# Kernel tuning notes

Measured on AMD Instinct MI355X. Metric: run time of the kernel, lower is better.

Reference implementation:

```python
import jax, jax.numpy as jnp
import numpy as np

NUM_HEADS = 10
LN_EPS = 1e-5


def setup_inputs() -> dict:
    key = jax.random.key(0)
    ks = jax.random.split(key, 6)
    N, D = 4096, 640  # in_dim == out_dim required by residual add
    x = jax.random.normal(ks[0], (N, D), dtype=jnp.float32)
    s = 1.0 / np.sqrt(D)
    Wq = jax.random.normal(ks[1], (D, D), dtype=jnp.float32) * s  # torch Linear weight [out,in]
    Wk = jax.random.normal(ks[2], (D, D), dtype=jnp.float32) * s
    Wv = jax.random.normal(ks[3], (D, D), dtype=jnp.float32) * s
    gamma = jnp.ones((D,), dtype=jnp.float32)
    beta = jnp.zeros((D,), dtype=jnp.float32)
    return {"x": x, "Wq": Wq, "Wk": Wk, "Wv": Wv, "gamma": gamma, "beta": beta}


def reference(x, Wq, Wk, Wv, gamma, beta):
    N, D = x.shape
    dk = D // NUM_HEADS
    Q = x @ Wq.T  # [N, D]
    K = x @ Wk.T
    V = x @ Wv.T
    # Faithful to source: raw reshapes (NOT transposes)
    Qh = Q.reshape(NUM_HEADS, N, dk)
    Kh = K.reshape(NUM_HEADS, N, dk).reshape(NUM_HEADS, dk, N)  # torch.reshape, not .mT
    Vh = V.reshape(NUM_HEADS, N, dk)
    # Faithful quirk: scale by sqrt(K.shape[2]) == sqrt(N)
    scale = np.float32(np.sqrt(N))
    wghts = jax.nn.softmax((Qh @ Kh) / scale, axis=-1)  # [H, N, N]
    values = wghts @ Vh  # [H, N, dk]
    values = values.reshape(N, NUM_HEADS * dk)  # raw reshape merge
    values = values + x  # residual
    # LayerNorm(out_dim), biased variance, eps=1e-5
    mean = jnp.mean(values, axis=-1, keepdims=True)
    var = jnp.mean(jnp.square(values - mean), axis=-1, keepdims=True)
    out = (values - mean) * jax.lax.rsqrt(var + LN_EPS) * gamma + beta
    return out
```

## Files before the change

kernel.cpp:

```cpp
#include <hip/hip_runtime.h>
#if __has_include(<hip/hip_fp8.h>)
#include <hip/hip_fp8.h>
#endif


typedef __bf16 bf16x8 __attribute__((ext_vector_type(8)));
typedef __bf16 bf16x4 __attribute__((ext_vector_type(4)));
typedef float  f32x4  __attribute__((ext_vector_type(4)));
typedef unsigned short u16x4 __attribute__((ext_vector_type(4)));
typedef unsigned int   u32x4 __attribute__((ext_vector_type(4)));

#define N_TOK   4096
#define D_MODEL 640
#define DK      64
#define HSLAB   (N_TOK * DK)
#define SQS 0.15014030f

#if __has_builtin(__builtin_amdgcn_exp2f)
#define EXP2(x) __builtin_amdgcn_exp2f(x)
#else
#define EXP2(x) exp2f(x)
#endif

__device__ __forceinline__ void stage16(const void* g, void* lds_uniform) {
    __builtin_amdgcn_global_load_lds(
        (const __attribute__((address_space(1))) unsigned int*)g,
        (__attribute__((address_space(3))) unsigned int*)lds_uniform, 16, 0, 0);
}

__device__ __forceinline__ u16x4 cvt4(f32x4 v) {
    return __builtin_bit_cast(u16x4, __builtin_convertvector(v, bf16x4));
}

__device__ __forceinline__ unsigned int pk_fp8(f32x4 v) {
#if __has_builtin(__builtin_amdgcn_cvt_pk_fp8_f32)
    int r = 0;
    r = __builtin_amdgcn_cvt_pk_fp8_f32(v[0], v[1], r, false);
    r = __builtin_amdgcn_cvt_pk_fp8_f32(v[2], v[3], r, true);
    return (unsigned int)r;
#else
    union { unsigned char b[4]; unsigned int u; } x;
    x.b[0] = __hip_fp8_e4m3(v[0]).__x;
    x.b[1] = __hip_fp8_e4m3(v[1]).__x;
    x.b[2] = __hip_fp8_e4m3(v[2]).__x;
    x.b[3] = __hip_fp8_e4m3(v[3]).__x;
    return x.u;
#endif
}

__global__ __launch_bounds__(256) void cvt_all(const float* __restrict__ x,
                                               const float* __restrict__ w0,
                                               const float* __restrict__ w1,
                                               const float* __restrict__ w2,
                                               unsigned short* __restrict__ xb,
                                               unsigned short* __restrict__ d0,
                                               unsigned short* __restrict__ d1,
                                               unsigned short* __restrict__ d2,
                                               f32x4* __restrict__ ltot4) {
    int i = blockIdx.x * 256 + threadIdx.x;
    if (i >= 962560) { ltot4[i - 962560] = (f32x4){0.f, 0.f, 0.f, 0.f}; return; }
    const float* s; unsigned short* d; int off; float scl = 1.0f;
    if (i < 655360) { s = x; d = xb; off = i; }
    else {
        int j = i - 655360;
        int w = j / 102400; off = j - w * 102400;
        s = (w == 0) ? w0 : (w == 1) ? w1 : w2;
        d = (w == 0) ? d0 : (w == 1) ? d1 : d2;
        if (w < 2) scl = SQS;
    }
    f32x4 v = ((const f32x4*)s)[off];
    v[0] *= scl; v[1] *= scl; v[2] *= scl; v[3] *= scl;
    ((u16x4*)d)[off] = cvt4(v);
}

__global__ __launch_bounds__(256, 2) void gemm_qkv(
    const unsigned short* __restrict__ xb,
    const unsigned short* __restrict__ wq,
    const unsigned short* __restrict__ wk,
    const unsigned short* __restrict__ wv,
    unsigned short* __restrict__ Qo,
    unsigned short* __restrict__ Ko,
    unsigned short* __restrict__ Vo) {
    const int mode = blockIdx.z;
    const unsigned short* W = (mode == 0) ? wq : (mode == 1) ? wk : wv;
    unsigned short*       C = (mode == 0) ? Qo : (mode == 1) ? Ko : Vo;
    const int m0 = blockIdx.y * 128;
    const int n0 = blockIdx.x * 128;

    __shared__ unsigned short As[4096];
    __shared__ unsigned short Bs[4096];

    const int tid  = threadIdx.x;
    const int lane = tid & 63;
    const int wave = tid >> 6;
    const int quad = lane >> 4, l16 = lane & 15;
    const int wm = (wave >> 1) * 64, wn = (wave & 1) * 64;
    const int swz3 = l16 & 3;

    f32x4 acc[4][4] = {};

    const int c0 = wave * 64 + lane, c1 = c0 + 256;
    const int r0 = c0 >> 2, u0 = ((c0 & 3) ^ (r0 & 3)) * 8;
    const int r1 = c1 >> 2, u1 = ((c1 & 3) ^ (r1 & 3)) * 8;
    const int lb0 = (wave * 64) * 8, lb1 = lb0 + 2048;

    for (int kt = 0; kt < D_MODEL; kt += 32) {
        __syncthreads();
        stage16(&xb[(size_t)(m0 + r0) * D_MODEL + kt + u0], As + lb0);
        stage16(&xb[(size_t)(m0 + r1) * D_MODEL + kt + u1], As + lb1);
        stage16(&W [(size_t)(n0 + r0) * D_MODEL + kt + u0], Bs + lb0);
        stage16(&W [(size_t)(n0 + r1) * D_MODEL + kt + u1], Bs + lb1);
        __syncthreads();

        bf16x8 af[4], bfr[4];
        for (int mi = 0; mi < 4; mi++)
            af[mi] = *(const bf16x8*)&As[(wm + mi * 16 + l16) * 32 + (quad ^ swz3) * 8];
        for (int ni = 0; ni < 4; ni++)
            bfr[ni] = *(const bf16x8*)&Bs[(wn + ni * 16 + l16) * 32 + (quad ^ swz3) * 8];
        for (int mi = 0; mi < 4; mi++)
            for (int ni = 0; ni < 4; ni++)
                acc[mi][ni] = __builtin_amdgcn_mfma_f32_16x16x32_bf16(af[mi], bfr[ni], acc[mi][ni], 0, 0, 0);
    }

    for (int mi = 0; mi < 4; mi++)
        for (int ni = 0; ni < 4; ni++) {
            u16x4 cv = cvt4(acc[mi][ni]);
            for (int r = 0; r < 4; r++) {
                int row = m0 + wm + mi * 16 + quad * 4 + r;
                int col = n0 + wn + ni * 16 + l16;
                C[(size_t)row * D_MODEL + col] = cv[r];
            }
        }
}

__global__ __launch_bounds__(256) void transpose_kv(
    const unsigned short* __restrict__ Kn, unsigned char* __restrict__ Kp8,
    const unsigned short* __restrict__ Vn, unsigned char* __restrict__ Vp8,
    const unsigned short* __restrict__ Qn, unsigned char* __restrict__ Qf8) {
    const int z = blockIdx.z;
    const int t = threadIdx.x;

    if (z >= 20) {
        const size_t base = (size_t)(z - 20) * HSLAB + blockIdx.x * 4096 + t * 16;
        bf16x8 v0 = *(const bf16x8*)&Qn[base];
        bf16x8 v1 = *(const bf16x8*)&Qn[base + 8];
        f32x4 a = {(float)v0[0], (float)v0[1], (float)v0[2], (float)v0[3]};
        f32x4 b = {(float)v0[4], (float)v0[5], (float)v0[6], (float)v0[7]};
        f32x4 c = {(float)v1[0], (float)v1[1], (float)v1[2], (float)v1[3]};
        f32x4 d = {(float)v1[4], (float)v1[5], (float)v1[6], (float)v1[7]};
        u32x4 o = {pk_fp8(a), pk_fp8(b), pk_fp8(c), pk_fp8(d)};
        *(u32x4*)&Qf8[base] = o;
        return;
    }

    __shared__ unsigned short T[64][66];
    const unsigned short* src; unsigned char* dst;
    int R, Cc, r0, c0;
    if (z < 10) { src = Kn; dst = Kp8; R = 64;   Cc = 4096; r0 = 0; c0 = blockIdx.x * 64; }
    else        { src = Vn; dst = Vp8; R = 4096; Cc = 64;   r0 = blockIdx.x * 64; c0 = 0; }
    const size_t hb = (size_t)(z % 10) * HSLAB;
    const int rr = t >> 3, c8 = (t & 7) * 8;

    for (int hf = 0; hf < 2; hf++) {
        int r = rr + hf * 32;
        bf16x8 v = *(const bf16x8*)&src[hb + (size_t)(r0 + r) * Cc + c0 + c8];
        for (int j = 0; j < 8; j++) T[r][c8 + j] = ((unsigned short*)&v)[j];
    }
    __syncthreads();
    const bf16x8 zz = {};
    for (int hf = 0; hf < 2; hf++) {
        int r = rr + hf * 32;
        *(bf16x8*)&((unsigned short*)src)[hb + (size_t)(r0 + r) * Cc + c0 + c8] = zz;
    }
    for (int hf = 0; hf < 2; hf++) {
        int oc = rr + hf * 32;
        f32x4 lo, hi;
        for (int j = 0; j < 4; j++) {
            lo[j] = __builtin_bit_cast(float, (unsigned int)T[c8 + j][oc] << 16);
            hi[j] = __builtin_bit_cast(float, (unsigned int)T[c8 + 4 + j][oc] << 16);
        }
        uint2 ov; ov.x = pk_fp8(lo); ov.y = pk_fp8(hi);
        size_t dcol = (z < 10) ? ((size_t)(c0 + oc) * 64 + r0 + c8)
                               : ((size_t)oc * 4096 + r0 + c8);
        *(uint2*)&dst[hb + dcol] = ov;
    }
}

__global__ __launch_bounds__(256, 4) void attn(
    const unsigned char* __restrict__ Qf8,
    const unsigned char* __restrict__ Kp8,
    const unsigned char* __restrict__ Vp8,
    float* __restrict__ vals,
    float* __restrict__ l_tot) {
    const int h  = blockIdx.x >> 5;
    const int qt = blockIdx.x & 31;
    const int ntile = (blockIdx.y == 2) ? 10 : 11;
    const int tile0 = blockIdx.y * 11;
    const int lane = threadIdx.x & 63;
    const int wave = threadIdx.x >> 6;
    const int quad = lane >> 4, l16 = lane & 15;
    const size_t hoff = (size_t)h * HSLAB;

    __shared__ unsigned char sm[32768];
    unsigned char* Kt = sm;
    unsigned char* Vt = sm + 8192;
    unsigned char* Pw = sm + 16384 + wave * 4096;

    const int qbase = qt * 128 + wave * 32;
    long qd[2][2];
    for (int g = 0; g < 2; g++) {
        const unsigned char* qp = Qf8 + hoff + (size_t)(qbase + g * 16 + l16) * 64 + quad * 8;
        qd[g][0] = *(const long*)(qp);
        qd[g][1] = *(const long*)(qp + 32);
    }

    f32x4 o[2][4] = {};
    f32x4 ol[2] = {};
    const long ONES8 = 0x3838383838383838L;

    const int cA = wave * 64 + lane, cB = cA + 256;
    const int kA = cA >> 2, uA = ((cA & 3) ^ (kA & 3)) << 4;
    const int kB = cB >> 2, uB = ((cB & 3) ^ (kB & 3)) << 4;
    const int dA = cA >> 3, wA = ((cA & 7) ^ (dA & 7)) << 4;
    const int dB = cB >> 3, wB = ((cB & 7) ^ (dB & 7)) << 4;

    for (int t = 0; t < ntile; t++) {
        const int keyb = (tile0 + t) << 7;
        __syncthreads();
        stage16(Kp8 + hoff + (size_t)(keyb + kA) * 64 + uA, Kt + wave * 1024);
        stage16(Kp8 + hoff + (size_t)(keyb + kB) * 64 + uB, Kt + 4096 + wave * 1024);
        stage16(Vp8 + hoff + (size_t)dA * N_TOK + keyb + wA, Vt + wave * 1024);
        stage16(Vp8 + hoff + (size_t)dB * N_TOK + keyb + wB, Vt + 4096 + wave * 1024);
        __syncthreads();

        for (int ni = 0; ni < 8; ni++) {
            const int keyloc = ni * 16 + l16;
            const unsigned char* kp = Kt + keyloc * 64 + (quad & 1) * 8;
            long a0 = *(const long*)(kp + ((((quad >> 1)    ) ^ (keyloc & 3)) << 4));
            long a1 = *(const long*)(kp + (((2 + (quad >> 1)) ^ (keyloc & 3)) << 4));
            for (int g = 0; g < 2; g++) {
                f32x4 s = {};
                s = __builtin_amdgcn_mfma_f32_16x16x32_fp8_fp8(a0, qd[g][0], s, 0, 0, 0);
                s = __builtin_amdgcn_mfma_f32_16x16x32_fp8_fp8(a1, qd[g][1], s, 0, 0, 0);
                f32x4 pv;
                for (int r = 0; r < 4; r++) pv[r] = EXP2(s[r]);
                *(unsigned int*)(Pw + (g * 16 + l16) * 128 +
                                 ((ni ^ (l16 & 7)) << 4) + quad * 4) = pk_fp8(pv);
            }
        }

        for (int ks = 0; ks < 4; ks++) {
            const int ub = (ks << 1) + (quad >> 1);
            long vf[4];
            for (int nd = 0; nd < 4; nd++) {
                const int dkl = nd * 16 + l16;
                vf[nd] = *(const long*)(Vt + dkl * 128 + ((ub ^ (dkl & 7)) << 4) + (quad & 1) * 8);
            }
            for (int g = 0; g < 2; g++) {
                long pf = *(const long*)(Pw + (g * 16 + l16) * 128 + ((ub ^ (l16 & 7)) << 4) + (quad & 1) * 8);
                ol[g] = __builtin_amdgcn_mfma_f32_16x16x32_fp8_fp8(pf, ONES8, ol[g], 0, 0, 0);
                for (int nd = 0; nd < 4; nd++)
                    o[g][nd] = __builtin_amdgcn_mfma_f32_16x16x32_fp8_fp8(pf, vf[nd], o[g][nd], 0, 0, 0);
            }
        }
    }

    if (l16 == 0)
        for (int g = 0; g < 2; g++)
            for (int r = 0; r < 4; r++)
                atomicAdd(&l_tot[(h << 12) + qbase + g * 16 + quad * 4 + r], ol[g][r]);

    for (int g = 0; g < 2; g++)
        for (int nd = 0; nd < 4; nd++)
            for (int r = 0; r < 4; r++) {
                int q = qbase + g * 16 + quad * 4 + r;
                atomicAdd(&vals[hoff + (size_t)q * DK + nd * 16 + l16], o[g][nd][r]);
            }
}

__global__ __launch_bounds__(256) void ln_kernel(
    const float* __restrict__ vals, const float* __restrict__ l_tot,
    const float* __restrict__ x,
    const float* __restrict__ gamma, const float* __restrict__ beta,
    float* __restrict__ out) {
    const int wave = threadIdx.x >> 6, lane = threadIdx.x & 63;
    const int row  = blockIdx.x * 4 + wave;
    const float* v  = vals + (size_t)row * D_MODEL;
    const float* xr = x    + (size_t)row * D_MODEL;

    float t[10];
    float s = 0.f;
    for (int i = 0; i < 10; i++) {
        float linv = 1.0f / l_tot[row * 10 + i];
        t[i] = v[lane + i * 64] * linv + xr[lane + i * 64];
        s += t[i];
    }
    for (int off = 32; off; off >>= 1) s += __shfl_xor(s, off, 64);
    float mean = s * (1.0f / 640.0f);
    float s2 = 0.f;
    for (int i = 0; i < 10; i++) { float d = t[i] - mean; s2 += d * d; }
    for (int off = 32; off; off >>= 1) s2 += __shfl_xor(s2, off, 64);
    float inv = rsqrtf(s2 * (1.0f / 640.0f) + 1e-5f);

    float* orow = out + (size_t)row * D_MODEL;
    for (int i = 0; i < 10; i++) {
        int c = lane + i * 64;
        orow[c] = (t[i] - mean) * inv * gamma[c] + beta[c];
    }
}

extern "C" void kernel_launch(void* const* d_in, const int* in_sizes, int n_in,
                              void* d_out, int out_size, void* d_ws, size_t ws_size,
                              hipStream_t stream) {
    const float* x     = (const float*)d_in[0];
    const float* Wq    = (const float*)d_in[1];
    const float* Wk    = (const float*)d_in[2];
    const float* Wv    = (const float*)d_in[3];
    const float* gamma = (const float*)d_in[4];
    const float* beta  = (const float*)d_in[5];
    float* out = (float*)d_out;

    char* ws = (char*)d_ws;
    unsigned short* xb  = (unsigned short*)(ws);
    unsigned char*  Qf8 = (unsigned char*)(ws);
    unsigned short* wqb = (unsigned short*)(ws + 5242880);
    unsigned short* wkb = (unsigned short*)(ws + 6062080);
    unsigned short* wvb = (unsigned short*)(ws + 6881280);
    unsigned short* Qn  = (unsigned short*)(ws + 7700480);
    unsigned char*  Kp8 = (unsigned char*)(ws + 12943360);
    unsigned char*  Vp8 = (unsigned char*)(ws + 18186240);
    unsigned short* Kn  = (unsigned short*)(ws + 23429120);
    unsigned short* Vn  = (unsigned short*)(ws + 28672000);
    float*          vals  = (float*)(ws + 23429120);
    float*          l_tot = (float*)(ws + 33914880);

    cvt_all<<<3800, 256, 0, stream>>>(x, Wq, Wk, Wv, xb, wqb, wkb, wvb,
                                      (f32x4*)l_tot);

    gemm_qkv<<<dim3(5, 32, 3), 256, 0, stream>>>(xb, wqb, wkb, wvb, Qn, Kn, Vn);

    transpose_kv<<<dim3(64, 1, 30), 256, 0, stream>>>(Kn, Kp8, Vn, Vp8, Qn, Qf8);

    attn<<<dim3(320, 3), 256, 0, stream>>>(Qf8, Kp8, Vp8, vals, l_tot);
    ln_kernel<<<1024, 256, 0, stream>>>(vals, l_tot, x, gamma, beta, out);
}
```

Baseline: 166.2 us.

## Re-layout K/V/P LDS tiles to drop XOR swizzle and add may_alias loads

Changes how K and V tiles are staged into LDS so each fragment read becomes a simple linear offset, replacing the XOR-swizzled addressing. The P buffer is also laid out by 8-byte column chunks, which turns the PV fragment reads into contiguous accesses. Loads now go through may_alias typedefs, and a block-wide barrier is added between the QK and PV phases. The aim is cheaper address arithmetic and possibly fewer LDS bank conflicts. The cost is an extra __syncthreads per tile and a risk of different bank-conflict behaviour.

```diff
diff --git a/kernel.cpp b/kernel.cpp
--- a/kernel.cpp
+++ b/kernel.cpp
@@ -9,6 +9,8 @@
 typedef float  f32x4  __attribute__((ext_vector_type(4)));
 typedef unsigned short u16x4 __attribute__((ext_vector_type(4)));
 typedef unsigned int   u32x4 __attribute__((ext_vector_type(4)));
+typedef long           la64  __attribute__((may_alias));
+typedef unsigned int   ua32  __attribute__((may_alias));
 
 #define N_TOK   4096
 #define D_MODEL 640
@@ -210,8 +212,8 @@
     long qd[2][2];
     for (int g = 0; g < 2; g++) {
         const unsigned char* qp = Qf8 + hoff + (size_t)(qbase + g * 16 + l16) * 64 + quad * 8;
-        qd[g][0] = *(const long*)(qp);
-        qd[g][1] = *(const long*)(qp + 32);
+        qd[g][0] = *(const la64*)(qp);
+        qd[g][1] = *(const la64*)(qp + 32);
     }
 
     f32x4 o[2][4] = {};
@@ -219,45 +221,46 @@
     const long ONES8 = 0x3838383838383838L;
 
     const int cA = wave * 64 + lane, cB = cA + 256;
-    const int kA = cA >> 2, uA = ((cA & 3) ^ (kA & 3)) << 4;
-    const int kB = cB >> 2, uB = ((cB & 3) ^ (kB & 3)) << 4;
-    const int dA = cA >> 3, wA = ((cA & 7) ^ (dA & 7)) << 4;
-    const int dB = cB >> 3, wB = ((cB & 7) ^ (dB & 7)) << 4;
+    const int kKeyA = ((cA >> 5) << 3) + (cA & 7), kCiA = (cA >> 3) & 3;
+    const int kKeyB = ((cB >> 5) << 3) + (cB & 7), kCiB = (cB >> 3) & 3;
+    const int vDkA  = ((cA >> 6) << 3) + (cA & 7), vCvA = (cA >> 3) & 7;
+    const int vDkB  = ((cB >> 6) << 3) + (cB & 7), vCvB = (cB >> 3) & 7;
+
+    const int kfb = (l16 >> 3) * 512 + (quad >> 1) * 128 + (l16 & 7) * 16 + (quad & 1) * 8;
+    const int vfb = (l16 >> 3) * 1024 + (quad >> 1) * 128 + (l16 & 7) * 16 + (quad & 1) * 8;
 
     for (int t = 0; t < ntile; t++) {
         const int keyb = (tile0 + t) << 7;
         __syncthreads();
-        stage16(Kp8 + hoff + (size_t)(keyb + kA) * 64 + uA, Kt + wave * 1024);
-        stage16(Kp8 + hoff + (size_t)(keyb + kB) * 64 + uB, Kt + 4096 + wave * 1024);
-        stage16(Vp8 + hoff + (size_t)dA * N_TOK + keyb + wA, Vt + wave * 1024);
-        stage16(Vp8 + hoff + (size_t)dB * N_TOK + keyb + wB, Vt + 4096 + wave * 1024);
+        stage16(Kp8 + hoff + (size_t)(keyb + kKeyA) * 64 + kCiA * 16, Kt + wave * 1024);
+        stage16(Kp8 + hoff + (size_t)(keyb + kKeyB) * 64 + kCiB * 16, Kt + 4096 + wave * 1024);
+        stage16(Vp8 + hoff + (size_t)vDkA * N_TOK + keyb + vCvA * 16, Vt + wave * 1024);
+        stage16(Vp8 + hoff + (size_t)vDkB * N_TOK + keyb + vCvB * 16, Vt + 4096 + wave * 1024);
         __syncthreads();
 
         for (int ni = 0; ni < 8; ni++) {
-            const int keyloc = ni * 16 + l16;
-            const unsigned char* kp = Kt + keyloc * 64 + (quad & 1) * 8;
-            long a0 = *(const long*)(kp + ((((quad >> 1)    ) ^ (keyloc & 3)) << 4));
-            long a1 = *(const long*)(kp + (((2 + (quad >> 1)) ^ (keyloc & 3)) << 4));
+            const unsigned char* kp = Kt + ni * 1024 + kfb;
+            long a0 = *(const la64*)(kp);
+            long a1 = *(const la64*)(kp + 256);
             for (int g = 0; g < 2; g++) {
                 f32x4 s = {};
                 s = __builtin_amdgcn_mfma_f32_16x16x32_fp8_fp8(a0, qd[g][0], s, 0, 0, 0);
                 s = __builtin_amdgcn_mfma_f32_16x16x32_fp8_fp8(a1, qd[g][1], s, 0, 0, 0);
                 f32x4 pv;
                 for (int r = 0; r < 4; r++) pv[r] = EXP2(s[r]);
-                *(unsigned int*)(Pw + (g * 16 + l16) * 128 +
-                                 ((ni ^ (l16 & 7)) << 4) + quad * 4) = pk_fp8(pv);
+                *(ua32*)(Pw + (ni * 2 + (quad >> 1)) * 256 +
+                         (g * 16 + l16) * 8 + (quad & 1) * 4) = pk_fp8(pv);
             }
         }
 
+        __syncthreads();
+
         for (int ks = 0; ks < 4; ks++) {
-            const int ub = (ks << 1) + (quad >> 1);
             long vf[4];
-            for (int nd = 0; nd < 4; nd++) {
-                const int dkl = nd * 16 + l16;
-                vf[nd] = *(const long*)(Vt + dkl * 128 + ((ub ^ (dkl & 7)) << 4) + (quad & 1) * 8);
-            }
+            for (int nd = 0; nd < 4; nd++)
+                vf[nd] = *(const la64*)(Vt + nd * 2048 + ks * 256 + vfb);
             for (int g = 0; g < 2; g++) {
-                long pf = *(const long*)(Pw + (g * 16 + l16) * 128 + ((ub ^ (l16 & 7)) << 4) + (quad & 1) * 8);
+                long pf = *(const la64*)(Pw + (ks * 4 + quad) * 256 + (g * 16 + l16) * 8);
                 ol[g] = __builtin_amdgcn_mfma_f32_16x16x32_fp8_fp8(pf, ONES8, ol[g], 0, 0, 0);
                 for (int nd = 0; nd < 4; nd++)
                     o[g][nd] = __builtin_amdgcn_mfma_f32_16x16x32_fp8_fp8(pf, vf[nd], o[g][nd], 0, 0, 0);
```

Result: faster. 162.6 us (-2.2%).
